# Optimization experiments

Measured on AMD Instinct MI355X. Metric: run time of the kernel, lower is better.

Reference implementation:

```python
import jax, jax.numpy as jnp
import numpy as np

NEG_INF = -1e30  # large negative instead of float('-inf') for fp16/bf16 safety in softmax


def setup_inputs() -> dict:
    key = jax.random.key(0)
    k1, k2, k3, k4 = jax.random.split(key, 4)
    B, T, C, H = 8, 2048, 768, 64
    x = jax.random.normal(k1, (B, T, C), dtype=jnp.float32)
    # nn.Linear(n_embd, head_size, bias=False): y = x @ W.T, W shape (head_size, n_embd)
    s = 1.0 / np.sqrt(C)
    Wk = jax.random.uniform(k2, (H, C), dtype=jnp.float32, minval=-s, maxval=s)
    Wq = jax.random.uniform(k3, (H, C), dtype=jnp.float32, minval=-s, maxval=s)
    Wv = jax.random.uniform(k4, (H, C), dtype=jnp.float32, minval=-s, maxval=s)
    return {"x": x, "Wk": Wk, "Wq": Wq, "Wv": Wv}


def reference(x, Wk, Wq, Wv):
    # x: [B,T,C]; Wk/Wq/Wv: [H,C]
    k = jnp.einsum('btc,hc->bth', x, Wk)  # [B,T,H]
    q = jnp.einsum('btc,hc->bth', x, Wq)
    v = jnp.einsum('btc,hc->bth', x, Wv)
    att = jnp.einsum('bqh,bkh->bqk', q, k)  # [B,T,T], NOTE: no 1/sqrt(H) scaling, faithful to source
    T = x.shape[1]
    causal = jnp.tril(jnp.ones((T, T), dtype=bool))
    att = jnp.where(causal, att, NEG_INF)
    att = jax.nn.softmax(att, axis=-1)
    out = jnp.einsum('bqk,bkh->bqh', att, v)  # [B,T,H]
    return out
```

## Files before the change

### kernel.cpp

```cpp
#include <hip/hip_runtime.h>
#include <hip/hip_bf16.h>
#include <stdint.h>

typedef float    f32x4  __attribute__((ext_vector_type(4)));
typedef float    f32x16 __attribute__((ext_vector_type(16)));
typedef short    s16x8  __attribute__((ext_vector_type(8)));
typedef uint32_t u32x4  __attribute__((ext_vector_type(4)));
typedef uint32_t u32x2  __attribute__((ext_vector_type(2)));

#define NB 8
#define NT 2048
#define NC 768
#define NH 64
#define LOG2E 1.4426950408889634f

__device__ __forceinline__ uint32_t f2bf1(float f) {
  union { float f; uint32_t u; } v; v.f = f;
  uint32_t u = v.u;
  return (u + 0x7fffu + ((u >> 16) & 1u)) >> 16;
}
__device__ __forceinline__ uint32_t packbf2(float lo, float hi) {
  union { __hip_bfloat162 h; uint32_t u; } c;
  c.h = __float22bfloat162_rn(float2{lo, hi});
  return c.u;
}
__device__ __forceinline__ float bf2f(short s) {
  union { float f; uint32_t u; } v; v.u = ((uint32_t)(uint16_t)s) << 16; return v.f;
}

__global__ __launch_bounds__(256) void wconv_kernel(
    const float* __restrict__ Wk, const float* __restrict__ Wq,
    const float* __restrict__ Wv, short* __restrict__ Wf)
{
  int f = blockIdx.x * 256 + threadIdx.x;
  int lane = f & 63;
  int rest = f >> 6;
  int ks = rest % 48;
  int nt = rest / 48;
  int col = lane & 31, half = lane >> 5;
  int n = nt * 32 + col;
  int k = ks * 16 + half * 8;
  const float* src;
  float sc = 1.0f;
  if (n < 64)       { src = Wq + (size_t)n * NC + k; sc = LOG2E; }
  else if (n < 128) { src = Wk + (size_t)(n - 64) * NC + k; }
  else              { src = Wv + (size_t)(n - 128) * NC + k; }
  f32x4 a = *(const f32x4*)src;
  f32x4 b = *(const f32x4*)(src + 4);
  u32x4 o = {packbf2(a[0] * sc, a[1] * sc), packbf2(a[2] * sc, a[3] * sc),
             packbf2(b[0] * sc, b[1] * sc), packbf2(b[2] * sc, b[3] * sc)};
  *(u32x4*)&Wf[(size_t)f * 8] = o;
}

__global__ __launch_bounds__(384, 2) void proj_kernel(
    const float* __restrict__ x, const short* __restrict__ Wf,
    short* __restrict__ qfb, short* __restrict__ kfb, short* __restrict__ vfb)
{
  __shared__ short ldsX[32 * 768];

  const int tid  = threadIdx.x;
  const int lane = tid & 63;
  const int w    = tid >> 6;
  const int col  = lane & 31;
  const int half = lane >> 5;
  const int tg   = blockIdx.x;
  const int t0   = tg * 32;

  {
#pragma unroll
    for (int i = 0; i < 8; ++i) {
      int c   = tid + 384 * i;
      int tok = c / 96, g = c % 96;
      const float* src = x + (size_t)(t0 + tok) * NC + g * 8;
      f32x4 a = *(const f32x4*)src;
      f32x4 d = *(const f32x4*)(src + 4);
      int swz = (g & ~7) | ((g ^ tok) & 7);
      u32x4 o = {packbf2(a[0], a[1]), packbf2(a[2], a[3]),
                 packbf2(d[0], d[1]), packbf2(d[2], d[3])};
      *(u32x4*)&ldsX[tok * 768 + swz * 8] = o;
    }
  }
  __syncthreads();

  f32x16 acc;
#pragma unroll
  for (int e = 0; e < 16; ++e) acc[e] = 0.f;

  const short* wbase = Wf + (((size_t)w * 48) << 9) + lane * 8;
  auto loadW = [&](int ks) -> s16x8 { return *(const s16x8*)(wbase + ((size_t)ks << 9)); };
  auto loadA = [&](int ks) -> s16x8 {
    int grp = ks * 2 + half;
    int swz = (grp & ~7) | ((grp ^ col) & 7);
    return *(const s16x8*)&ldsX[col * 768 + swz * 8];
  };
  {
    s16x8 wA = loadW(0), aA = loadA(0), wB, aB;
#pragma unroll
    for (int ks = 0; ks < 48; ks += 2) {
      wB = loadW(ks + 1); aB = loadA(ks + 1);
      acc = __builtin_amdgcn_mfma_f32_32x32x16_bf16(aA, wA, acc, 0, 0, 0);
      if (ks + 2 < 48) { wA = loadW(ks + 2); aA = loadA(ks + 2); }
      acc = __builtin_amdgcn_mfma_f32_32x32x16_bf16(aB, wB, acc, 0, 0, 0);
    }
  }
  __syncthreads();

  short* scr = ldsX + w * 1088;
  const size_t base = (size_t)tg * 2048;
  if (w < 4) {
#pragma unroll
    for (int r = 0; r < 16; ++r) {
      int rd = (r & 3) + 8 * (r >> 2) + 4 * half;
      scr[rd * 34 + col] = (short)f2bf1(acc[r]);
    }
    short* dst = (w < 2) ? qfb : kfb;
    int ksBase = (w & 1) * 2;
#pragma unroll
    for (int j = 0; j < 2; ++j) {
      s16x8 v = *(const s16x8*)&scr[col * 34 + j * 16 + half * 8];
      *(s16x8*)&dst[base + (ksBase + j) * 512 + lane * 8] = v;
    }
  } else {
#pragma unroll
    for (int r = 0; r < 16; ++r) {
      int rd = (r & 3) + 8 * (r >> 2) + 4 * half;
      scr[col * 34 + rd] = (short)f2bf1(acc[r]);
    }
    int hh = w - 4;
#pragma unroll
    for (int j = 0; j < 2; ++j) {
      s16x8 v = *(const s16x8*)&scr[col * 34 + j * 16 + half * 8];
      *(s16x8*)&vfb[base + (hh * 2 + j) * 512 + lane * 8] = v;
    }
  }
}

__global__ __launch_bounds__(512, 2) void attn_kernel(
    const short* __restrict__ qfb, const short* __restrict__ kfb,
    const short* __restrict__ vfb, float* __restrict__ out)
{
  __shared__ short ldsOb[8 * 32 * 72];
  __shared__ float ldsM[8 * 32];
  __shared__ float ldsL[8 * 32];

  const int tid  = threadIdx.x;
  const int lane = tid & 63;
  const int w8   = tid >> 6;
  const int col  = lane & 31;
  const int half = lane >> 5;
  const int b    = blockIdx.x & 7;
  const int qt   = 63 - (blockIdx.x >> 3);
  const int nT   = qt + 1;

  s16x8 qf[4];
  {
    const short* qp = qfb + (size_t)(b * 64 + qt) * 2048 + lane * 8;
#pragma unroll
    for (int ks = 0; ks < 4; ++ks) qf[ks] = *(const s16x8*)(qp + ks * 512);
  }
  const short* kfp = kfb + (size_t)b * 64 * 2048 + lane * 8;
  const short* vfp = vfb + (size_t)b * 64 * 2048 + lane * 8;

  f32x16 oacc[2];
#pragma unroll
  for (int i = 0; i < 2; ++i)
#pragma unroll
    for (int e = 0; e < 16; ++e) oacc[i][e] = 0.f;
  float m = -1e30f, l = 0.f;

  s16x8 kA[4], vA[4], kB[4], vB[4];
  auto loadT = [&](s16x8* dk, s16x8* dv, int t) {
    const short* kp = kfp + (size_t)t * 2048;
    const short* vp = vfp + (size_t)t * 2048;
#pragma unroll
    for (int i = 0; i < 4; ++i) {
      dk[i] = *(const s16x8*)(kp + i * 512);
      dv[i] = *(const s16x8*)(vp + i * 512);
    }
  };
  auto body = [&](s16x8* ck, s16x8* cv, int t) {
    f32x16 s;
#pragma unroll
    for (int e = 0; e < 16; ++e) s[e] = 0.f;
#pragma unroll
    for (int ks = 0; ks < 4; ++ks)
      s = __builtin_amdgcn_mfma_f32_32x32x16_bf16(ck[ks], qf[ks], s, 0, 0, 0);

    if (t == qt) {
#pragma unroll
      for (int r = 0; r < 16; ++r) {
        int rd = (r & 3) + 8 * (r >> 2) + 4 * half;
        if (rd > col) s[r] = -1e30f;
      }
    }
    float vmax = s[0];
#pragma unroll
    for (int r = 1; r < 16; ++r) vmax = fmaxf(vmax, s[r]);
    vmax = fmaxf(vmax, __shfl_xor(vmax, 32));
    float mn    = fmaxf(m, vmax);
    float alpha = exp2f(m - mn);
    float p[16];
    float rs = 0.f;
#pragma unroll
    for (int r = 0; r < 16; ++r) { p[r] = exp2f(s[r] - mn); rs += p[r]; }
    rs += __shfl_xor(rs, 32);
    l = l * alpha + rs;
    m = mn;
#pragma unroll
    for (int i = 0; i < 2; ++i)
#pragma unroll
      for (int e = 0; e < 16; ++e) oacc[i][e] *= alpha;

    uint32_t pw[8];
#pragma unroll
    for (int i = 0; i < 8; ++i) pw[i] = packbf2(p[2 * i], p[2 * i + 1]);
#pragma unroll
    for (int kc = 0; kc < 2; ++kc) {
      uint32_t s0 = half ? pw[4 * kc]     : pw[4 * kc + 2];
      uint32_t s1 = half ? pw[4 * kc + 1] : pw[4 * kc + 3];
      uint32_t r0 = __shfl_xor(s0, 32);
      uint32_t r1 = __shfl_xor(s1, 32);
      uint32_t w0 = half ? r0 : pw[4 * kc];
      uint32_t w1 = half ? r1 : pw[4 * kc + 1];
      uint32_t w2 = half ? pw[4 * kc + 2] : r0;
      uint32_t w3 = half ? pw[4 * kc + 3] : r1;
      union { u32x4 u; s16x8 v; } pf;
      pf.u = (u32x4){w0, w1, w2, w3};
#pragma unroll
      for (int ht = 0; ht < 2; ++ht)
        oacc[ht] = __builtin_amdgcn_mfma_f32_32x32x16_bf16(cv[ht * 2 + kc], pf.v, oacc[ht], 0, 0, 0);
    }
  };

  int t = w8;
  if (t < nT) loadT(kA, vA, t);
  if (t + 8 < nT) loadT(kB, vB, t + 8);
  for (; t + 8 < nT; t += 16) {
    body(kA, vA, t);
    if (t + 16 < nT) loadT(kA, vA, t + 16);
    body(kB, vB, t + 8);
    if (t + 24 < nT) loadT(kB, vB, t + 24);
  }
  if (t < nT) body(kA, vA, t);

  if (half == 0) { ldsM[w8 * 32 + col] = m; ldsL[w8 * 32 + col] = l; }
#pragma unroll
  for (int ht = 0; ht < 2; ++ht)
#pragma unroll
    for (int u = 0; u < 4; ++u) {
      int h = ht * 32 + 8 * u + 4 * half;
      u32x2 pk = {packbf2(oacc[ht][4 * u + 0], oacc[ht][4 * u + 1]),
                  packbf2(oacc[ht][4 * u + 2], oacc[ht][4 * u + 3])};
      *(u32x2*)&ldsOb[(w8 * 32 + col) * 72 + h] = pk;
    }
  __syncthreads();

  {
    const int rr = tid >> 4;
    const int h0 = (tid & 15) * 4;
    float M = -1e30f;
#pragma unroll
    for (int s = 0; s < 8; ++s) M = fmaxf(M, ldsM[s * 32 + rr]);
    float Ls = 0.f;
    float o[4] = {0.f, 0.f, 0.f, 0.f};
#pragma unroll
    for (int s = 0; s < 8; ++s) {
      float cf = exp2f(ldsM[s * 32 + rr] - M);
      Ls += cf * ldsL[s * 32 + rr];
      const short* row = &ldsOb[(s * 32 + rr) * 72 + h0];
#pragma unroll
      for (int j = 0; j < 4; ++j) o[j] += cf * bf2f(row[j]);
    }
    float inv = 1.0f / Ls;
    float* ob = out + (size_t)(b * NT + qt * 32 + rr) * NH + h0;
    *(f32x4*)ob = (f32x4){o[0] * inv, o[1] * inv, o[2] * inv, o[3] * inv};
  }
}

extern "C" void kernel_launch(void* const* d_in, const int* in_sizes, int n_in,
                              void* d_out, int out_size, void* d_ws, size_t ws_size,
                              hipStream_t stream) {
  const float* x  = (const float*)d_in[0];
  const float* Wk = (const float*)d_in[1];
  const float* Wq = (const float*)d_in[2];
  const float* Wv = (const float*)d_in[3];
  float* out = (float*)d_out;

  char* ws = (char*)d_ws;
  short* Wf  = (short*)(ws);
  short* qfb = (short*)(ws + (512 << 10));
  short* kfb = (short*)(ws + (512 << 10) + (2 << 20));
  short* vfb = (short*)(ws + (512 << 10) + (4 << 20));

  hipLaunchKernelGGL(wconv_kernel, dim3(72),  dim3(256), 0, stream, Wk, Wq, Wv, Wf);
  hipLaunchKernelGGL(proj_kernel,  dim3(512), dim3(384), 0, stream, x, Wf, qfb, kfb, vfb);
  hipLaunchKernelGGL(attn_kernel,  dim3(512), dim3(512), 0, stream, qfb, kfb, vfb, out);
}
```

Baseline: 110.6 us.

## Use persistent attention blocks with atomic work queue; deepen projection load pipeline

The attention kernel becomes persistent with a grid of 320 blocks. Blocks take causal query-tile work items from a global atomic counter, heaviest tiles first, which is meant to balance the triangular workload across CUs. The weight-convert kernel resets the counter on each launch. The projection kernel's K loop now uses a 4-deep register ring of prefetched loads instead of double-buffering, to hide more load latency. The persistent scheme adds atomic and barrier overhead per item and uses more registers in the projection kernel.

New measurement: 116.2 us. +5.1%, slower.

```diff
diff --git a/kernel.cpp b/kernel.cpp
--- a/kernel.cpp
+++ b/kernel.cpp
@@ -13,6 +13,8 @@
 #define NC 768
 #define NH 64
 #define LOG2E 1.4426950408889634f
+#define ATTN_GRID 320
+#define ATTN_ITEMS 512
 
 __device__ __forceinline__ uint32_t f2bf1(float f) {
   union { float f; uint32_t u; } v; v.f = f;
@@ -30,8 +32,9 @@
 
 __global__ __launch_bounds__(256) void wconv_kernel(
     const float* __restrict__ Wk, const float* __restrict__ Wq,
-    const float* __restrict__ Wv, short* __restrict__ Wf)
+    const float* __restrict__ Wv, short* __restrict__ Wf, uint32_t* __restrict__ ctr)
 {
+  if (blockIdx.x == 0 && threadIdx.x == 0) *ctr = ATTN_GRID;
   int f = blockIdx.x * 256 + threadIdx.x;
   int lane = f & 63;
   int rest = f >> 6;
@@ -94,13 +97,14 @@
     return *(const s16x8*)&ldsX[col * 768 + swz * 8];
   };
   {
-    s16x8 wA = loadW(0), aA = loadA(0), wB, aB;
-#pragma unroll
-    for (int ks = 0; ks < 48; ks += 2) {
-      wB = loadW(ks + 1); aB = loadA(ks + 1);
-      acc = __builtin_amdgcn_mfma_f32_32x32x16_bf16(aA, wA, acc, 0, 0, 0);
-      if (ks + 2 < 48) { wA = loadW(ks + 2); aA = loadA(ks + 2); }
-      acc = __builtin_amdgcn_mfma_f32_32x32x16_bf16(aB, wB, acc, 0, 0, 0);
+    s16x8 wb[4], ab[4];
+#pragma unroll
+    for (int i = 0; i < 4; ++i) { wb[i] = loadW(i); ab[i] = loadA(i); }
+#pragma unroll
+    for (int ks = 0; ks < 48; ++ks) {
+      int c = ks & 3;
+      acc = __builtin_amdgcn_mfma_f32_32x32x16_bf16(ab[c], wb[c], acc, 0, 0, 0);
+      if (ks + 4 < 48) { wb[c] = loadW(ks + 4); ab[c] = loadA(ks + 4); }
     }
   }
   __syncthreads();
@@ -137,143 +141,154 @@
 
 __global__ __launch_bounds__(512, 2) void attn_kernel(
     const short* __restrict__ qfb, const short* __restrict__ kfb,
-    const short* __restrict__ vfb, float* __restrict__ out)
+    const short* __restrict__ vfb, float* __restrict__ out,
+    uint32_t* __restrict__ ctr)
 {
   __shared__ short ldsOb[8 * 32 * 72];
   __shared__ float ldsM[8 * 32];
   __shared__ float ldsL[8 * 32];
+  __shared__ int   nextItem;
 
   const int tid  = threadIdx.x;
   const int lane = tid & 63;
   const int w8   = tid >> 6;
   const int col  = lane & 31;
   const int half = lane >> 5;
-  const int b    = blockIdx.x & 7;
-  const int qt   = 63 - (blockIdx.x >> 3);
-  const int nT   = qt + 1;
-
-  s16x8 qf[4];
-  {
-    const short* qp = qfb + (size_t)(b * 64 + qt) * 2048 + lane * 8;
-#pragma unroll
-    for (int ks = 0; ks < 4; ++ks) qf[ks] = *(const s16x8*)(qp + ks * 512);
-  }
-  const short* kfp = kfb + (size_t)b * 64 * 2048 + lane * 8;
-  const short* vfp = vfb + (size_t)b * 64 * 2048 + lane * 8;
-
-  f32x16 oacc[2];
-#pragma unroll
-  for (int i = 0; i < 2; ++i)
-#pragma unroll
-    for (int e = 0; e < 16; ++e) oacc[i][e] = 0.f;
-  float m = -1e30f, l = 0.f;
-
-  s16x8 kA[4], vA[4], kB[4], vB[4];
-  auto loadT = [&](s16x8* dk, s16x8* dv, int t) {
-    const short* kp = kfp + (size_t)t * 2048;
-    const short* vp = vfp + (size_t)t * 2048;
-#pragma unroll
-    for (int i = 0; i < 4; ++i) {
-      dk[i] = *(const s16x8*)(kp + i * 512);
-      dv[i] = *(const s16x8*)(vp + i * 512);
-    }
-  };
-  auto body = [&](s16x8* ck, s16x8* cv, int t) {
-    f32x16 s;
-#pragma unroll
-    for (int e = 0; e < 16; ++e) s[e] = 0.f;
-#pragma unroll
-    for (int ks = 0; ks < 4; ++ks)
-      s = __builtin_amdgcn_mfma_f32_32x32x16_bf16(ck[ks], qf[ks], s, 0, 0, 0);
-
-    if (t == qt) {
-#pragma unroll
-      for (int r = 0; r < 16; ++r) {
-        int rd = (r & 3) + 8 * (r >> 2) + 4 * half;
-        if (rd > col) s[r] = -1e30f;
-      }
-    }
-    float vmax = s[0];
-#pragma unroll
-    for (int r = 1; r < 16; ++r) vmax = fmaxf(vmax, s[r]);
-    vmax = fmaxf(vmax, __shfl_xor(vmax, 32));
-    float mn    = fmaxf(m, vmax);
-    float alpha = exp2f(m - mn);
-    float p[16];
-    float rs = 0.f;
-#pragma unroll
-    for (int r = 0; r < 16; ++r) { p[r] = exp2f(s[r] - mn); rs += p[r]; }
-    rs += __shfl_xor(rs, 32);
-    l = l * alpha + rs;
-    m = mn;
+
+  int item = blockIdx.x;
+  while (item < ATTN_ITEMS) {
+    const int b  = item & 7;
+    const int qt = 63 - (item >> 3);
+    const int nT = qt + 1;
+
+    s16x8 qf[4];
+    {
+      const short* qp = qfb + (size_t)(b * 64 + qt) * 2048 + lane * 8;
+#pragma unroll
+      for (int ks = 0; ks < 4; ++ks) qf[ks] = *(const s16x8*)(qp + ks * 512);
+    }
+    const short* kfp = kfb + (size_t)b * 64 * 2048 + lane * 8;
+    const short* vfp = vfb + (size_t)b * 64 * 2048 + lane * 8;
+
+    f32x16 oacc[2];
 #pragma unroll
     for (int i = 0; i < 2; ++i)
 #pragma unroll
-      for (int e = 0; e < 16; ++e) oacc[i][e] *= alpha;
-
-    uint32_t pw[8];
-#pragma unroll
-    for (int i = 0; i < 8; ++i) pw[i] = packbf2(p[2 * i], p[2 * i + 1]);
-#pragma unroll
-    for (int kc = 0; kc < 2; ++kc) {
-      uint32_t s0 = half ? pw[4 * kc]     : pw[4 * kc + 2];
-      uint32_t s1 = half ? pw[4 * kc + 1] : pw[4 * kc + 3];
-      uint32_t r0 = __shfl_xor(s0, 32);
-      uint32_t r1 = __shfl_xor(s1, 32);
-      uint32_t w0 = half ? r0 : pw[4 * kc];
-      uint32_t w1 = half ? r1 : pw[4 * kc + 1];
-      uint32_t w2 = half ? pw[4 * kc + 2] : r0;
-      uint32_t w3 = half ? pw[4 * kc + 3] : r1;
-      union { u32x4 u; s16x8 v; } pf;
-      pf.u = (u32x4){w0, w1, w2, w3};
-#pragma unroll
-      for (int ht = 0; ht < 2; ++ht)
-        oacc[ht] = __builtin_amdgcn_mfma_f32_32x32x16_bf16(cv[ht * 2 + kc], pf.v, oacc[ht], 0, 0, 0);
-    }
-  };
-
-  int t = w8;
-  if (t < nT) loadT(kA, vA, t);
-  if (t + 8 < nT) loadT(kB, vB, t + 8);
-  for (; t + 8 < nT; t += 16) {
-    body(kA, vA, t);
-    if (t + 16 < nT) loadT(kA, vA, t + 16);
-    body(kB, vB, t + 8);
-    if (t + 24 < nT) loadT(kB, vB, t + 24);
-  }
-  if (t < nT) body(kA, vA, t);
-
-  if (half == 0) { ldsM[w8 * 32 + col] = m; ldsL[w8 * 32 + col] = l; }
-#pragma unroll
-  for (int ht = 0; ht < 2; ++ht)
-#pragma unroll
-    for (int u = 0; u < 4; ++u) {
-      int h = ht * 32 + 8 * u + 4 * half;
-      u32x2 pk = {packbf2(oacc[ht][4 * u + 0], oacc[ht][4 * u + 1]),
-                  packbf2(oacc[ht][4 * u + 2], oacc[ht][4 * u + 3])};
-      *(u32x2*)&ldsOb[(w8 * 32 + col) * 72 + h] = pk;
-    }
-  __syncthreads();
-
-  {
-    const int rr = tid >> 4;
-    const int h0 = (tid & 15) * 4;
-    float M = -1e30f;
-#pragma unroll
-    for (int s = 0; s < 8; ++s) M = fmaxf(M, ldsM[s * 32 + rr]);
-    float Ls = 0.f;
-    float o[4] = {0.f, 0.f, 0.f, 0.f};
-#pragma unroll
-    for (int s = 0; s < 8; ++s) {
-      float cf = exp2f(ldsM[s * 32 + rr] - M);
-      Ls += cf * ldsL[s * 32 + rr];
-      const short* row = &ldsOb[(s * 32 + rr) * 72 + h0];
-#pragma unroll
-      for (int j = 0; j < 4; ++j) o[j] += cf * bf2f(row[j]);
-    }
-    float inv = 1.0f / Ls;
-    float* ob = out + (size_t)(b * NT + qt * 32 + rr) * NH + h0;
-    *(f32x4*)ob = (f32x4){o[0] * inv, o[1] * inv, o[2] * inv, o[3] * inv};
+      for (int e = 0; e < 16; ++e) oacc[i][e] = 0.f;
+    float m = -1e30f, l = 0.f;
+
+    s16x8 kA[4], vA[4], kB[4], vB[4];
+    auto loadT = [&](s16x8* dk, s16x8* dv, int t) {
+      const short* kp = kfp + (size_t)t * 2048;
+      const short* vp = vfp + (size_t)t * 2048;
+#pragma unroll
+      for (int i = 0; i < 4; ++i) {
+        dk[i] = *(const s16x8*)(kp + i * 512);
+        dv[i] = *(const s16x8*)(vp + i * 512);
+      }
+    };
+    auto body = [&](s16x8* ck, s16x8* cv, int t) {
+      f32x16 s;
+#pragma unroll
+      for (int e = 0; e < 16; ++e) s[e] = 0.f;
+#pragma unroll
+      for (int ks = 0; ks < 4; ++ks)
+        s = __builtin_amdgcn_mfma_f32_32x32x16_bf16(ck[ks], qf[ks], s, 0, 0, 0);
+
+      if (t == qt) {
+#pragma unroll
+        for (int r = 0; r < 16; ++r) {
+          int rd = (r & 3) + 8 * (r >> 2) + 4 * half;
+          if (rd > col) s[r] = -1e30f;
+        }
+      }
+      float vmax = s[0];
+#pragma unroll
+      for (int r = 1; r < 16; ++r) vmax = fmaxf(vmax, s[r]);
+      vmax = fmaxf(vmax, __shfl_xor(vmax, 32));
+      float mn    = fmaxf(m, vmax);
+      float alpha = exp2f(m - mn);
+      float p[16];
+      float rs = 0.f;
+#pragma unroll
+      for (int r = 0; r < 16; ++r) { p[r] = exp2f(s[r] - mn); rs += p[r]; }
+      rs += __shfl_xor(rs, 32);
+      l = l * alpha + rs;
+      m = mn;
+#pragma unroll
+      for (int i = 0; i < 2; ++i)
+#pragma unroll
+        for (int e = 0; e < 16; ++e) oacc[i][e] *= alpha;
+
+      uint32_t pw[8];
+#pragma unroll
+      for (int i = 0; i < 8; ++i) pw[i] = packbf2(p[2 * i], p[2 * i + 1]);
+#pragma unroll
+      for (int kc = 0; kc < 2; ++kc) {
+        uint32_t s0 = half ? pw[4 * kc]     : pw[4 * kc + 2];
+        uint32_t s1 = half ? pw[4 * kc + 1] : pw[4 * kc + 3];
+        uint32_t r0 = __shfl_xor(s0, 32);
+        uint32_t r1 = __shfl_xor(s1, 32);
+        uint32_t w0 = half ? r0 : pw[4 * kc];
+        uint32_t w1 = half ? r1 : pw[4 * kc + 1];
+        uint32_t w2 = half ? pw[4 * kc + 2] : r0;
+        uint32_t w3 = half ? pw[4 * kc + 3] : r1;
+        union { u32x4 u; s16x8 v; } pf;
+        pf.u = (u32x4){w0, w1, w2, w3};
+#pragma unroll
+        for (int ht = 0; ht < 2; ++ht)
+          oacc[ht] = __builtin_amdgcn_mfma_f32_32x32x16_bf16(cv[ht * 2 + kc], pf.v, oacc[ht], 0, 0, 0);
+      }
+    };
+
+    int t = w8;
+    if (t < nT) loadT(kA, vA, t);
+    if (t + 8 < nT) loadT(kB, vB, t + 8);
+    for (; t + 8 < nT; t += 16) {
+      body(kA, vA, t);
+      if (t + 16 < nT) loadT(kA, vA, t + 16);
+      body(kB, vB, t + 8);
+      if (t + 24 < nT) loadT(kB, vB, t + 24);
+    }
+    if (t < nT) body(kA, vA, t);
+
+    if (half == 0) { ldsM[w8 * 32 + col] = m; ldsL[w8 * 32 + col] = l; }
+#pragma unroll
+    for (int ht = 0; ht < 2; ++ht)
+#pragma unroll
+      for (int u = 0; u < 4; ++u) {
+        int h = ht * 32 + 8 * u + 4 * half;
+        u32x2 pk = {packbf2(oacc[ht][4 * u + 0], oacc[ht][4 * u + 1]),
+                    packbf2(oacc[ht][4 * u + 2], oacc[ht][4 * u + 3])};
+        *(u32x2*)&ldsOb[(w8 * 32 + col) * 72 + h] = pk;
+      }
+    __syncthreads();
+
+    {
+      const int rr = tid >> 4;
+      const int h0 = (tid & 15) * 4;
+      float M = -1e30f;
+#pragma unroll
+      for (int s = 0; s < 8; ++s) M = fmaxf(M, ldsM[s * 32 + rr]);
+      float Ls = 0.f;
+      float o[4] = {0.f, 0.f, 0.f, 0.f};
+#pragma unroll
+      for (int s = 0; s < 8; ++s) {
+        float cf = exp2f(ldsM[s * 32 + rr] - M);
+        Ls += cf * ldsL[s * 32 + rr];
+        const short* row = &ldsOb[(s * 32 + rr) * 72 + h0];
+#pragma unroll
+        for (int j = 0; j < 4; ++j) o[j] += cf * bf2f(row[j]);
+      }
+      float inv = 1.0f / Ls;
+      float* ob = out + (size_t)(b * NT + qt * 32 + rr) * NH + h0;
+      *(f32x4*)ob = (f32x4){o[0] * inv, o[1] * inv, o[2] * inv, o[3] * inv};
+    }
+
+    __syncthreads();
+    if (tid == 0) nextItem = (int)atomicAdd(ctr, 1u);
+    __syncthreads();
+    item = nextItem;
   }
 }
 
@@ -291,8 +306,9 @@
   short* qfb = (short*)(ws + (512 << 10));
   short* kfb = (short*)(ws + (512 << 10) + (2 << 20));
   short* vfb = (short*)(ws + (512 << 10) + (4 << 20));
-
-  hipLaunchKernelGGL(wconv_kernel, dim3(72),  dim3(256), 0, stream, Wk, Wq, Wv, Wf);
+  uint32_t* ctr = (uint32_t*)(ws + (512 << 10) + (6 << 20));
+
+  hipLaunchKernelGGL(wconv_kernel, dim3(72),  dim3(256), 0, stream, Wk, Wq, Wv, Wf, ctr);
   hipLaunchKernelGGL(proj_kernel,  dim3(512), dim3(384), 0, stream, x, Wf, qfb, kfb, vfb);
-  hipLaunchKernelGGL(attn_kernel,  dim3(512), dim3(512), 0, stream, qfb, kfb, vfb, out);
-}
+  hipLaunchKernelGGL(attn_kernel,  dim3(ATTN_GRID), dim3(512), 0, stream, qfb, kfb, vfb, out, ctr);
+}
```
